# Kernel tuning notes

Measured on AMD Instinct MI355X. Metric: run time of the kernel, lower is better.

## Reference

```python
import jax, jax.numpy as jnp
import numpy as np

B, H, S, D = 1, 16, 4096, 64

def setup_inputs() -> dict:
    key = jax.random.key(0)
    kq, kk, kv = jax.random.split(key, 3)
    return {
        "query": jax.random.normal(kq, (B, H, S, D), dtype=jnp.float32),
        "key": jax.random.normal(kk, (B, H, S, D), dtype=jnp.float32),
        "value": jax.random.normal(kv, (B, H, S, D), dtype=jnp.float32),
    }

def reference(query, key, value):
    # qk: [B,H,S,S] materialized score matrix (unfused, as in original)
    qk = jnp.einsum("bhqd,bhkd->bhqk", query, key)
    attn = jax.nn.softmax(qk, axis=-1)
    # dropout_p = 0.0 -> identity
    out = jnp.einsum("bhqk,bhkd->bhqd", attn, value)
    return out
```

## Files before the change

kernel.cpp:

```cpp
#include <hip/hip_runtime.h>
#include <math.h>


#define HH 16
#define SS 4096
#define DDm 64
#define WAVES 8
#define QBW 32
#define QB (WAVES * QBW)
#define KB 64
#define NTL (SS / KB)
#define LDP 72

typedef __attribute__((ext_vector_type(2))) _Float16 half2_t;
typedef __attribute__((ext_vector_type(4))) _Float16 half4_t;
typedef __attribute__((ext_vector_type(8))) _Float16 half8_t;
typedef __attribute__((ext_vector_type(16))) float f32x16;

union H8 { half2_t h2[4]; half8_t v; };
union FU { float f; unsigned u; };
union HU { half2_t h; unsigned u; };

__device__ inline unsigned asu(float x){ FU c; c.f=x; return c.u; }
__device__ inline float    asf(unsigned x){ FU c; c.u=x; return c.f; }
__device__ inline unsigned h2u(half2_t x){ HU c; c.h=x; return c.u; }
__device__ inline half2_t  u2h(unsigned x){ HU c; c.u=x; return c.h; }
__device__ inline half2_t  pk2(float a, float b){ half2_t h; h[0]=(_Float16)a; h[1]=(_Float16)b; return h; }

#if __has_builtin(__builtin_amdgcn_permlane32_swap)
#define HAVE_PL32 1
typedef __attribute__((ext_vector_type(2))) unsigned uint2_t;
__device__ inline uint2_t pl32(unsigned a, unsigned b){
  return __builtin_amdgcn_permlane32_swap(a, b, false, false);
}
#endif

#if __has_builtin(__builtin_amdgcn_exp2f)
#define EXP2F(x) __builtin_amdgcn_exp2f(x)
#else
#define EXP2F(x) exp2f(x)
#endif
#define L2E 1.44269504088896f

#define WAITVM(n) asm volatile("s_waitcnt vmcnt(" #n ")" ::: "memory")

__device__ __forceinline__ void gload16(const void* g, void* l) {
  __builtin_amdgcn_global_load_lds(
      (const __attribute__((address_space(1))) unsigned int*)g,
      (__attribute__((address_space(3))) unsigned int*)l, 16, 0, 0);
}

__global__ __launch_bounds__(256)
void prepack(const float* __restrict__ K, const float* __restrict__ V,
             _Float16* __restrict__ Kh, _Float16* __restrict__ Vth) {
  const int g = blockIdx.x;
  const int tid = threadIdx.x;
  if (g < 2048) {
    const int gt = g * 256 + tid;
    const int dg = gt & 7, r = (gt >> 3) & 63, t = (gt >> 9) & 63, h = gt >> 15;
    const float* src = K + ((size_t)(h * SS + t * 64 + r)) * DDm + dg * 8;
    float4 a = *(const float4*)src;
    float4 b = *(const float4*)(src + 4);
    H8 w;
    w.h2[0] = pk2(a.x, a.y); w.h2[1] = pk2(a.z, a.w);
    w.h2[2] = pk2(b.x, b.y); w.h2[3] = pk2(b.z, b.w);
    *(half8_t*)(Kh + (size_t)(h * 64 + t) * 4096 + (dg * 64 + r) * 8) = w.v;
  } else {
    const int gt = (g - 2048) * 256 + tid;
    const int dr = gt & 63, kg = (gt >> 6) & 7, t = (gt >> 9) & 63, h = gt >> 15;
    const float* src = V + ((size_t)(h * SS + t * 64 + kg * 8)) * DDm + dr;
    H8 w;
#pragma unroll
    for (int j = 0; j < 4; ++j)
      w.h2[j] = pk2(src[(2 * j) * DDm], src[(2 * j + 1) * DDm]);
    *(half8_t*)(Vth + (size_t)(h * 64 + t) * 4096 + (kg * 64 + dr) * 8) = w.v;
  }
}

__global__ __launch_bounds__(512, 2)
void attn_main(const float* __restrict__ Q, const _Float16* __restrict__ Kh,
               const _Float16* __restrict__ Vth, float* __restrict__ O) {
  __shared__ __align__(16) _Float16 Kbuf[3][4096];
  __shared__ __align__(16) _Float16 Vbuf[3][4096];

  const int tid  = threadIdx.x;
  const int lane = tid & 63;
  const int lo5  = lane & 31;
  const int hi   = lane >> 5;
  const int wv   = tid >> 6;

  const int lid  = blockIdx.x;
  const int head = 2 * (lid & 7) + ((lid >> 3) & 1);
  const int qt   = lid >> 4;
  const int qbase = qt * QB + wv * QBW;
  const size_t hoff = (size_t)head * SS * DDm;

  H8 qf[4];
  {
    const float* qp = Q + hoff + (size_t)(qbase + lo5) * DDm;
#pragma unroll
    for (int ds = 0; ds < 4; ++ds) {
      float4 a = *(const float4*)(qp + 16 * ds + 8 * hi);
      float4 b = *(const float4*)(qp + 16 * ds + 8 * hi + 4);
      qf[ds].h2[0] = pk2(a.x, a.y); qf[ds].h2[1] = pk2(a.z, a.w);
      qf[ds].h2[2] = pk2(b.x, b.y); qf[ds].h2[3] = pk2(b.z, b.w);
    }
  }

  const _Float16* kt0 = Kh + (size_t)head * 64 * 4096;
  const _Float16* vt0 = Vth + (size_t)head * 64 * 4096;

  f32x16 acc[2];
#pragma unroll
  for (int nt = 0; nt < 2; ++nt)
#pragma unroll
    for (int r = 0; r < 16; ++r) acc[nt][r] = 0.f;
  float m_run = -INFINITY, l_run = 0.f;

  gload16(kt0 + (size_t)tid * 8, &Kbuf[0][wv * 512]);
  gload16(vt0 + (size_t)tid * 8, &Vbuf[0][wv * 512]);
  gload16(kt0 + 4096 + (size_t)tid * 8, &Kbuf[1][wv * 512]);
  gload16(vt0 + 4096 + (size_t)tid * 8, &Vbuf[1][wv * 512]);

  int bc = 0;
  for (int t = 0; t < NTL; ++t) {
    if (t < NTL - 1) { WAITVM(2); } else { WAITVM(0); }
    __builtin_amdgcn_s_barrier();
    __builtin_amdgcn_sched_barrier(0);
    if (t + 2 < NTL) {
      int bi = bc + 2; if (bi >= 3) bi -= 3;
      gload16(kt0 + (size_t)(t + 2) * 4096 + (size_t)tid * 8, &Kbuf[bi][wv * 512]);
      gload16(vt0 + (size_t)(t + 2) * 4096 + (size_t)tid * 8, &Vbuf[bi][wv * 512]);
    }

    half8_t kf[2][4];
#pragma unroll
    for (int s = 0; s < 2; ++s)
#pragma unroll
      for (int ds = 0; ds < 4; ++ds)
        kf[s][ds] = *(const half8_t*)&Kbuf[bc][((ds * 2 + hi) * 64 + 32 * s + lo5) * 8];
    half8_t vfr[2][2][2];
#pragma unroll
    for (int s = 0; s < 2; ++s)
#pragma unroll
      for (int sp = 0; sp < 2; ++sp)
#pragma unroll
        for (int nt = 0; nt < 2; ++nt)
          vfr[s][sp][nt] = *(const half8_t*)&Vbuf[bc][(((s * 2 + sp) * 2 + hi) * 64 + nt * 32 + lo5) * 8];

#pragma unroll
    for (int s = 0; s < 2; ++s) {
      f32x16 st;
#pragma unroll
      for (int r = 0; r < 16; ++r) st[r] = 0.f;
#pragma unroll
      for (int ds = 0; ds < 4; ++ds)
        st = __builtin_amdgcn_mfma_f32_32x32x16_f16(kf[s][ds], qf[ds].v, st, 0, 0, 0);

      float a0 = fmaxf(st[0], st[1]),   a1 = fmaxf(st[2], st[3]);
      float a2 = fmaxf(st[4], st[5]),   a3 = fmaxf(st[6], st[7]);
      float a4 = fmaxf(st[8], st[9]),   a5 = fmaxf(st[10], st[11]);
      float a6 = fmaxf(st[12], st[13]), a7 = fmaxf(st[14], st[15]);
      float b0 = fmaxf(a0, a1), b1 = fmaxf(a2, a3);
      float b2 = fmaxf(a4, a5), b3 = fmaxf(a6, a7);
      float tmax = fmaxf(fmaxf(b0, b1), fmaxf(b2, b3));
#if HAVE_PL32
      { uint2_t pr = pl32(asu(tmax), asu(tmax)); tmax = fmaxf(asf(pr[0]), asf(pr[1])); }
#else
      tmax = fmaxf(tmax, __shfl_xor(tmax, 32, 64));
#endif
      if (__any(tmax > m_run + 8.f)) {
        float mnew = fmaxf(m_run, tmax);
        float corr = EXP2F((m_run - mnew) * L2E);
        m_run = mnew; l_run *= corr;
#pragma unroll
        for (int r = 0; r < 16; ++r) {
          const int qr = (r & 3) + 8 * (r >> 2) + 4 * hi;
          float cf = asf(__builtin_amdgcn_ds_bpermute(qr << 2, asu(corr)));
          acc[0][r] *= cf; acc[1][r] *= cf;
        }
      }

      const float mt = m_run * L2E;
      float p[16];
      float s0 = 0.f, s1 = 0.f, s2 = 0.f, s3 = 0.f;
#pragma unroll
      for (int r = 0; r < 16; r += 4) {
        p[r]     = EXP2F(__builtin_fmaf(st[r],     L2E, -mt)); s0 += p[r];
        p[r + 1] = EXP2F(__builtin_fmaf(st[r + 1], L2E, -mt)); s1 += p[r + 1];
        p[r + 2] = EXP2F(__builtin_fmaf(st[r + 2], L2E, -mt)); s2 += p[r + 2];
        p[r + 3] = EXP2F(__builtin_fmaf(st[r + 3], L2E, -mt)); s3 += p[r + 3];
      }
      float lsum = (s0 + s1) + (s2 + s3);
#if HAVE_PL32
      { uint2_t pr = pl32(asu(lsum), asu(lsum)); lsum = asf(pr[0]) + asf(pr[1]); }
#else
      lsum += __shfl_xor(lsum, 32, 64);
#endif
      l_run += lsum;

      H8 pa[2];
#pragma unroll
      for (int step = 0; step < 2; ++step) {
        const int b = 8 * step;
        half2_t x0 = pk2(p[b + 0], p[b + 1]);
        half2_t x1 = pk2(p[b + 2], p[b + 3]);
        half2_t y0 = pk2(p[b + 4], p[b + 5]);
        half2_t y1 = pk2(p[b + 6], p[b + 7]);
#if HAVE_PL32
        uint2_t sA = pl32(h2u(x0), h2u(y0));
        uint2_t sB = pl32(h2u(x1), h2u(y1));
        pa[step].h2[0] = u2h(sA[0]); pa[step].h2[1] = u2h(sB[0]);
        pa[step].h2[2] = u2h(sA[1]); pa[step].h2[3] = u2h(sB[1]);
#else
        half2_t sx0 = u2h(__shfl_xor(h2u(x0), 32, 64));
        half2_t sx1 = u2h(__shfl_xor(h2u(x1), 32, 64));
        half2_t sy0 = u2h(__shfl_xor(h2u(y0), 32, 64));
        half2_t sy1 = u2h(__shfl_xor(h2u(y1), 32, 64));
        pa[step].h2[0] = hi ? sy0 : x0;  pa[step].h2[1] = hi ? sy1 : x1;
        pa[step].h2[2] = hi ? y0 : sx0;  pa[step].h2[3] = hi ? y1 : sx1;
#endif
      }
#pragma unroll
      for (int step = 0; step < 2; ++step)
#pragma unroll
        for (int nt = 0; nt < 2; ++nt)
          acc[nt] = __builtin_amdgcn_mfma_f32_32x32x16_f16(pa[step].v, vfr[s][step][nt], acc[nt], 0, 0, 0);
    }

    bc += 1; if (bc >= 3) bc = 0;
  }

  const float invl = 1.f / l_run;
#pragma unroll
  for (int r = 0; r < 16; ++r) {
    const int qr = (r & 3) + 8 * (r >> 2) + 4 * hi;
    float il = asf(__builtin_amdgcn_ds_bpermute(qr << 2, asu(invl)));
    float* op = O + hoff + (size_t)(qbase + qr) * DDm + lo5;
    op[0]  = acc[0][r] * il;
    op[32] = acc[1][r] * il;
  }
}

__global__ __launch_bounds__(512, 2)
void attn_fwd_fb(const float* __restrict__ Q, const float* __restrict__ K,
                 const float* __restrict__ V, float* __restrict__ O) {
  __shared__ __align__(16) _Float16 Klds[2][KB][LDP];
  __shared__ __align__(16) _Float16 Vt  [2][DDm][LDP];

  const int tid  = threadIdx.x;
  const int lane = tid & 63;
  const int lo5  = lane & 31;
  const int hi   = lane >> 5;

  const int lid  = blockIdx.x;
  const int head = 2 * (lid & 7) + ((lid >> 3) & 1);
  const int qt   = lid >> 4;
  const int qbase = qt * QB + (tid >> 6) * QBW;
  const size_t hoff = (size_t)head * SS * DDm;

  H8 qf[4];
  {
    const float* qp = Q + hoff + (size_t)(qbase + lo5) * DDm;
#pragma unroll
    for (int ds = 0; ds < 4; ++ds) {
      float4 a = *(const float4*)(qp + 16 * ds + 8 * hi);
      float4 b = *(const float4*)(qp + 16 * ds + 8 * hi + 4);
      qf[ds].h2[0] = pk2(a.x, a.y); qf[ds].h2[1] = pk2(a.z, a.w);
      qf[ds].h2[2] = pk2(b.x, b.y); qf[ds].h2[3] = pk2(b.z, b.w);
    }
  }

  const int krow = tid >> 3, kc8 = (tid & 7) * 8;
  const int vd = tid & 63, vk8 = (tid >> 6) * 8;

  float4 ka, kb; float va[8];
  auto issue = [&](int t) {
    const float* kp = K + hoff + (size_t)(t * KB + krow) * DDm + kc8;
    ka = *(const float4*)kp;
    kb = *(const float4*)(kp + 4);
    const float* vp = V + hoff + (size_t)(t * KB + vk8) * DDm + vd;
#pragma unroll
    for (int j = 0; j < 8; ++j) va[j] = vp[j * DDm];
  };
  auto wstage = [&](int buf) {
    H8 kw;
    kw.h2[0] = pk2(ka.x, ka.y); kw.h2[1] = pk2(ka.z, ka.w);
    kw.h2[2] = pk2(kb.x, kb.y); kw.h2[3] = pk2(kb.z, kb.w);
    *(half8_t*)&Klds[buf][krow][kc8] = kw.v;
    H8 vw;
#pragma unroll
    for (int j = 0; j < 4; ++j) vw.h2[j] = pk2(va[2 * j], va[2 * j + 1]);
    *(half8_t*)&Vt[buf][vd][vk8] = vw.v;
  };

  f32x16 acc[2];
#pragma unroll
  for (int nt = 0; nt < 2; ++nt)
#pragma unroll
    for (int r = 0; r < 16; ++r) acc[nt][r] = 0.f;
  float m_run = -INFINITY, l_run = 0.f;

  issue(0); wstage(0); __syncthreads();

  for (int t = 0; t < NTL; ++t) {
    const int cur = t & 1;
    if (t + 1 < NTL) issue(t + 1);

#pragma unroll
    for (int s = 0; s < 2; ++s) {
      const int rs = 32 * s;
      f32x16 st;
#pragma unroll
      for (int r = 0; r < 16; ++r) st[r] = 0.f;
#pragma unroll
      for (int ds = 0; ds < 4; ++ds) {
        half8_t af = *(const half8_t*)&Klds[cur][rs + lo5][16 * ds + 8 * hi];
        st = __builtin_amdgcn_mfma_f32_32x32x16_f16(af, qf[ds].v, st, 0, 0, 0);
      }
      float tmax = st[0];
#pragma unroll
      for (int r = 1; r < 16; ++r) tmax = fmaxf(tmax, st[r]);
#if HAVE_PL32
      { uint2_t pr = pl32(asu(tmax), asu(tmax)); tmax = fmaxf(asf(pr[0]), asf(pr[1])); }
#else
      tmax = fmaxf(tmax, __shfl_xor(tmax, 32, 64));
#endif
      if (__any(tmax > m_run + 8.f)) {
        float mnew = fmaxf(m_run, tmax);
        float corr = __expf(m_run - mnew);
        m_run = mnew; l_run *= corr;
#pragma unroll
        for (int r = 0; r < 16; ++r) {
          const int qr = (r & 3) + 8 * (r >> 2) + 4 * hi;
          float cf = asf(__builtin_amdgcn_ds_bpermute(qr << 2, asu(corr)));
          acc[0][r] *= cf; acc[1][r] *= cf;
        }
      }
      float p[16]; float lsum = 0.f;
#pragma unroll
      for (int r = 0; r < 16; ++r) { p[r] = __expf(st[r] - m_run); lsum += p[r]; }
#if HAVE_PL32
      { uint2_t pr = pl32(asu(lsum), asu(lsum)); lsum = asf(pr[0]) + asf(pr[1]); }
#else
      lsum += __shfl_xor(lsum, 32, 64);
#endif
      l_run += lsum;
      H8 pa[2];
#pragma unroll
      for (int step = 0; step < 2; ++step) {
        const int b = 8 * step;
        half2_t x0 = pk2(p[b + 0], p[b + 1]);
        half2_t x1 = pk2(p[b + 2], p[b + 3]);
        half2_t y0 = pk2(p[b + 4], p[b + 5]);
        half2_t y1 = pk2(p[b + 6], p[b + 7]);
#if HAVE_PL32
        uint2_t sA = pl32(h2u(x0), h2u(y0));
        uint2_t sB = pl32(h2u(x1), h2u(y1));
        pa[step].h2[0] = u2h(sA[0]); pa[step].h2[1] = u2h(sB[0]);
        pa[step].h2[2] = u2h(sA[1]); pa[step].h2[3] = u2h(sB[1]);
#else
        half2_t sx0 = u2h(__shfl_xor(h2u(x0), 32, 64));
        half2_t sx1 = u2h(__shfl_xor(h2u(x1), 32, 64));
        half2_t sy0 = u2h(__shfl_xor(h2u(y0), 32, 64));
        half2_t sy1 = u2h(__shfl_xor(h2u(y1), 32, 64));
        pa[step].h2[0] = hi ? sy0 : x0;  pa[step].h2[1] = hi ? sy1 : x1;
        pa[step].h2[2] = hi ? y0 : sx0;  pa[step].h2[3] = hi ? y1 : sx1;
#endif
      }
#pragma unroll
      for (int step = 0; step < 2; ++step)
#pragma unroll
        for (int nt = 0; nt < 2; ++nt) {
          half8_t vb = *(const half8_t*)&Vt[cur][32 * nt + lo5][rs + 16 * step + 8 * hi];
          acc[nt] = __builtin_amdgcn_mfma_f32_32x32x16_f16(pa[step].v, vb, acc[nt], 0, 0, 0);
        }
    }

    __syncthreads();
    if (t + 1 < NTL) wstage((t + 1) & 1);
    __syncthreads();
  }

  const float invl = 1.f / l_run;
#pragma unroll
  for (int r = 0; r < 16; ++r) {
    const int qr = (r & 3) + 8 * (r >> 2) + 4 * hi;
    float il = asf(__builtin_amdgcn_ds_bpermute(qr << 2, asu(invl)));
    float* op = O + hoff + (size_t)(qbase + qr) * DDm + lo5;
    op[0]  = acc[0][r] * il;
    op[32] = acc[1][r] * il;
  }
}

extern "C" void kernel_launch(void* const* d_in, const int* in_sizes, int n_in,
                              void* d_out, int out_size, void* d_ws, size_t ws_size,
                              hipStream_t stream) {
  const float* Q = (const float*)d_in[0];
  const float* K = (const float*)d_in[1];
  const float* V = (const float*)d_in[2];
  float* O = (float*)d_out;
  const size_t need = (size_t)2 * HH * SS * DDm * sizeof(_Float16);
  if (ws_size >= need) {
    _Float16* Kh  = (_Float16*)d_ws;
    _Float16* Vth = Kh + (size_t)HH * SS * DDm;
    prepack<<<dim3(4096), dim3(256), 0, stream>>>(K, V, Kh, Vth);
    attn_main<<<dim3(256), dim3(512), 0, stream>>>(Q, Kh, Vth, O);
  } else {
    attn_fwd_fb<<<dim3(256), dim3(512), 0, stream>>>(Q, K, V, O);
  }
}
```

Before: 115.2 us.

## Load K/V fragments directly from global into registers, drop LDS staging

Removes the shared-memory triple buffer and barriers from the main attention kernel. Each wave now loads its K and V MFMA fragments straight from the prepacked global buffers into registers, double-buffered across tiles. Blocks shrink from 512 to 256 threads and the grid doubles to keep the same query coverage. Each wave reading the full K/V tiles itself multiplies global/L2 traffic, and holding two register buffers raises register pressure.

```diff
diff --git a/kernel.cpp b/kernel.cpp
--- a/kernel.cpp
+++ b/kernel.cpp
@@ -5,15 +5,11 @@
 #define HH 16
 #define SS 4096
 #define DDm 64
-#define WAVES 8
-#define QBW 32
-#define QB (WAVES * QBW)
 #define KB 64
 #define NTL (SS / KB)
 #define LDP 72
 
 typedef __attribute__((ext_vector_type(2))) _Float16 half2_t;
-typedef __attribute__((ext_vector_type(4))) _Float16 half4_t;
 typedef __attribute__((ext_vector_type(8))) _Float16 half8_t;
 typedef __attribute__((ext_vector_type(16))) float f32x16;
 
@@ -41,14 +37,6 @@
 #define EXP2F(x) exp2f(x)
 #endif
 #define L2E 1.44269504088896f
-
-#define WAITVM(n) asm volatile("s_waitcnt vmcnt(" #n ")" ::: "memory")
-
-__device__ __forceinline__ void gload16(const void* g, void* l) {
-  __builtin_amdgcn_global_load_lds(
-      (const __attribute__((address_space(1))) unsigned int*)g,
-      (__attribute__((address_space(3))) unsigned int*)l, 16, 0, 0);
-}
 
 __global__ __launch_bounds__(256)
 void prepack(const float* __restrict__ K, const float* __restrict__ V,
@@ -77,12 +65,9 @@
   }
 }
 
-__global__ __launch_bounds__(512, 2)
+__global__ __launch_bounds__(256, 2)
 void attn_main(const float* __restrict__ Q, const _Float16* __restrict__ Kh,
                const _Float16* __restrict__ Vth, float* __restrict__ O) {
-  __shared__ __align__(16) _Float16 Kbuf[3][4096];
-  __shared__ __align__(16) _Float16 Vbuf[3][4096];
-
   const int tid  = threadIdx.x;
   const int lane = tid & 63;
   const int lo5  = lane & 31;
@@ -92,7 +77,7 @@
   const int lid  = blockIdx.x;
   const int head = 2 * (lid & 7) + ((lid >> 3) & 1);
   const int qt   = lid >> 4;
-  const int qbase = qt * QB + wv * QBW;
+  const int qbase = qt * 128 + wv * 32;
   const size_t hoff = (size_t)head * SS * DDm;
 
   H8 qf[4];
@@ -107,8 +92,27 @@
     }
   }
 
-  const _Float16* kt0 = Kh + (size_t)head * 64 * 4096;
-  const _Float16* vt0 = Vth + (size_t)head * 64 * 4096;
+  const _Float16* ktb = Kh + (size_t)head * 64 * 4096 + (hi * 64 + lo5) * 8;
+  const _Float16* vtb = Vth + (size_t)head * 64 * 4096 + (hi * 64 + lo5) * 8;
+
+  auto loadK = [&](int t, half8_t (&k)[8]) {
+    const _Float16* p = ktb + (size_t)t * 4096;
+#pragma unroll
+    for (int s = 0; s < 2; ++s)
+#pragma unroll
+      for (int ds = 0; ds < 4; ++ds)
+        k[s * 4 + ds] = *(const half8_t*)(p + (ds * 128 + 32 * s) * 8);
+  };
+  auto loadV = [&](int t, half8_t (&v)[8]) {
+    const _Float16* p = vtb + (size_t)t * 4096;
+#pragma unroll
+    for (int s = 0; s < 2; ++s)
+#pragma unroll
+      for (int sp = 0; sp < 2; ++sp)
+#pragma unroll
+        for (int nt = 0; nt < 2; ++nt)
+          v[s * 4 + sp * 2 + nt] = *(const half8_t*)(p + ((s * 2 + sp) * 128 + nt * 32) * 8);
+  };
 
   f32x16 acc[2];
 #pragma unroll
@@ -117,37 +121,7 @@
     for (int r = 0; r < 16; ++r) acc[nt][r] = 0.f;
   float m_run = -INFINITY, l_run = 0.f;
 
-  gload16(kt0 + (size_t)tid * 8, &Kbuf[0][wv * 512]);
-  gload16(vt0 + (size_t)tid * 8, &Vbuf[0][wv * 512]);
-  gload16(kt0 + 4096 + (size_t)tid * 8, &Kbuf[1][wv * 512]);
-  gload16(vt0 + 4096 + (size_t)tid * 8, &Vbuf[1][wv * 512]);
-
-  int bc = 0;
-  for (int t = 0; t < NTL; ++t) {
-    if (t < NTL - 1) { WAITVM(2); } else { WAITVM(0); }
-    __builtin_amdgcn_s_barrier();
-    __builtin_amdgcn_sched_barrier(0);
-    if (t + 2 < NTL) {
-      int bi = bc + 2; if (bi >= 3) bi -= 3;
-      gload16(kt0 + (size_t)(t + 2) * 4096 + (size_t)tid * 8, &Kbuf[bi][wv * 512]);
-      gload16(vt0 + (size_t)(t + 2) * 4096 + (size_t)tid * 8, &Vbuf[bi][wv * 512]);
-    }
-
-    half8_t kf[2][4];
-#pragma unroll
-    for (int s = 0; s < 2; ++s)
-#pragma unroll
-      for (int ds = 0; ds < 4; ++ds)
-        kf[s][ds] = *(const half8_t*)&Kbuf[bc][((ds * 2 + hi) * 64 + 32 * s + lo5) * 8];
-    half8_t vfr[2][2][2];
-#pragma unroll
-    for (int s = 0; s < 2; ++s)
-#pragma unroll
-      for (int sp = 0; sp < 2; ++sp)
-#pragma unroll
-        for (int nt = 0; nt < 2; ++nt)
-          vfr[s][sp][nt] = *(const half8_t*)&Vbuf[bc][(((s * 2 + sp) * 2 + hi) * 64 + nt * 32 + lo5) * 8];
-
+  auto compute = [&](half8_t (&k)[8], half8_t (&v)[8]) {
 #pragma unroll
     for (int s = 0; s < 2; ++s) {
       f32x16 st;
@@ -155,7 +129,7 @@
       for (int r = 0; r < 16; ++r) st[r] = 0.f;
 #pragma unroll
       for (int ds = 0; ds < 4; ++ds)
-        st = __builtin_amdgcn_mfma_f32_32x32x16_f16(kf[s][ds], qf[ds].v, st, 0, 0, 0);
+        st = __builtin_amdgcn_mfma_f32_32x32x16_f16(k[s * 4 + ds], qf[ds].v, st, 0, 0, 0);
 
       float a0 = fmaxf(st[0], st[1]),   a1 = fmaxf(st[2], st[3]);
       float a2 = fmaxf(st[4], st[5]),   a3 = fmaxf(st[6], st[7]);
@@ -225,10 +199,17 @@
       for (int step = 0; step < 2; ++step)
 #pragma unroll
         for (int nt = 0; nt < 2; ++nt)
-          acc[nt] = __builtin_amdgcn_mfma_f32_32x32x16_f16(pa[step].v, vfr[s][step][nt], acc[nt], 0, 0, 0);
+          acc[nt] = __builtin_amdgcn_mfma_f32_32x32x16_f16(pa[step].v, v[s * 4 + step * 2 + nt], acc[nt], 0, 0, 0);
     }
-
-    bc += 1; if (bc >= 3) bc = 0;
+  };
+
+  half8_t kA[8], vA[8], kB[8], vB[8];
+  loadK(0, kA); loadV(0, vA);
+  for (int t = 0; t < NTL; t += 2) {
+    loadK(t + 1, kB); loadV(t + 1, vB);
+    compute(kA, vA);
+    if (t + 2 < NTL) { loadK(t + 2, kA); loadV(t + 2, vA); }
+    compute(kB, vB);
   }
 
   const float invl = 1.f / l_run;
@@ -256,7 +237,7 @@
   const int lid  = blockIdx.x;
   const int head = 2 * (lid & 7) + ((lid >> 3) & 1);
   const int qt   = lid >> 4;
-  const int qbase = qt * QB + (tid >> 6) * QBW;
+  const int qbase = qt * 256 + (tid >> 6) * 32;
   const size_t hoff = (size_t)head * SS * DDm;
 
   H8 qf[4];
@@ -405,7 +386,7 @@
     _Float16* Kh  = (_Float16*)d_ws;
     _Float16* Vth = Kh + (size_t)HH * SS * DDm;
     prepack<<<dim3(4096), dim3(256), 0, stream>>>(K, V, Kh, Vth);
-    attn_main<<<dim3(256), dim3(512), 0, stream>>>(Q, Kh, Vth, O);
+    attn_main<<<dim3(512), dim3(256), 0, stream>>>(Q, Kh, Vth, O);
   } else {
     attn_fwd_fb<<<dim3(256), dim3(512), 0, stream>>>(Q, K, V, O);
   }
```

Result: slower. 125.3 us (+8.8%).

## Split KV sequence across two blocks per query tile and merge partials

Applied to the files above, without the earlier changes.

Adds a split-KV (flash-decoding style) path where each query tile is handled by two blocks, each covering half the key/value sequence, writing unnormalized accumulators plus running max and sum to workspace. A new merge kernel combines the two halves with log-sum-exp rescaling. This doubles the grid from 256 to 512 blocks to fill more compute units, at the cost of an extra kernel launch and partial-result traffic through global memory. The fp32 fallback kernel is removed, so no path runs when the workspace is too small.

```diff
diff --git a/kernel.cpp b/kernel.cpp
--- a/kernel.cpp
+++ b/kernel.cpp
@@ -5,15 +5,12 @@
 #define HH 16
 #define SS 4096
 #define DDm 64
-#define WAVES 8
-#define QBW 32
-#define QB (WAVES * QBW)
 #define KB 64
 #define NTL (SS / KB)
+#define NTLH 32
 #define LDP 72
 
 typedef __attribute__((ext_vector_type(2))) _Float16 half2_t;
-typedef __attribute__((ext_vector_type(4))) _Float16 half4_t;
 typedef __attribute__((ext_vector_type(8))) _Float16 half8_t;
 typedef __attribute__((ext_vector_type(16))) float f32x16;
 
@@ -78,8 +75,9 @@
 }
 
 __global__ __launch_bounds__(512, 2)
-void attn_main(const float* __restrict__ Q, const _Float16* __restrict__ Kh,
-               const _Float16* __restrict__ Vth, float* __restrict__ O) {
+void attn_split(const float* __restrict__ Q, const _Float16* __restrict__ Kh,
+                const _Float16* __restrict__ Vth, float* __restrict__ Pacc,
+                float* __restrict__ Pml) {
   __shared__ __align__(16) _Float16 Kbuf[3][4096];
   __shared__ __align__(16) _Float16 Vbuf[3][4096];
 
@@ -91,8 +89,206 @@
 
   const int lid  = blockIdx.x;
   const int head = 2 * (lid & 7) + ((lid >> 3) & 1);
+  const int rest = lid >> 4;
+  const int qt   = rest & 15;
+  const int half = rest >> 4;
+  const int qbase = qt * 256 + wv * 32;
+  const size_t hoff = (size_t)head * SS * DDm;
+
+  H8 qf[4];
+  {
+    const float* qp = Q + hoff + (size_t)(qbase + lo5) * DDm;
+#pragma unroll
+    for (int ds = 0; ds < 4; ++ds) {
+      float4 a = *(const float4*)(qp + 16 * ds + 8 * hi);
+      float4 b = *(const float4*)(qp + 16 * ds + 8 * hi + 4);
+      qf[ds].h2[0] = pk2(a.x, a.y); qf[ds].h2[1] = pk2(a.z, a.w);
+      qf[ds].h2[2] = pk2(b.x, b.y); qf[ds].h2[3] = pk2(b.z, b.w);
+    }
+  }
+
+  const _Float16* kt0 = Kh + (size_t)head * 64 * 4096 + (size_t)half * NTLH * 4096;
+  const _Float16* vt0 = Vth + (size_t)head * 64 * 4096 + (size_t)half * NTLH * 4096;
+
+  f32x16 acc[2];
+#pragma unroll
+  for (int nt = 0; nt < 2; ++nt)
+#pragma unroll
+    for (int r = 0; r < 16; ++r) acc[nt][r] = 0.f;
+  float m_run = -INFINITY, l_run = 0.f;
+
+  gload16(kt0 + (size_t)tid * 8, &Kbuf[0][wv * 512]);
+  gload16(vt0 + (size_t)tid * 8, &Vbuf[0][wv * 512]);
+  gload16(kt0 + 4096 + (size_t)tid * 8, &Kbuf[1][wv * 512]);
+  gload16(vt0 + 4096 + (size_t)tid * 8, &Vbuf[1][wv * 512]);
+
+  int bc = 0;
+  for (int t = 0; t < NTLH; ++t) {
+    if (t < NTLH - 1) { WAITVM(2); } else { WAITVM(0); }
+    __builtin_amdgcn_s_barrier();
+    __builtin_amdgcn_sched_barrier(0);
+    if (t + 2 < NTLH) {
+      int bi = bc + 2; if (bi >= 3) bi -= 3;
+      gload16(kt0 + (size_t)(t + 2) * 4096 + (size_t)tid * 8, &Kbuf[bi][wv * 512]);
+      gload16(vt0 + (size_t)(t + 2) * 4096 + (size_t)tid * 8, &Vbuf[bi][wv * 512]);
+    }
+
+    half8_t kf[2][4];
+#pragma unroll
+    for (int s = 0; s < 2; ++s)
+#pragma unroll
+      for (int ds = 0; ds < 4; ++ds)
+        kf[s][ds] = *(const half8_t*)&Kbuf[bc][((ds * 2 + hi) * 64 + 32 * s + lo5) * 8];
+    half8_t vfr[2][2][2];
+#pragma unroll
+    for (int s = 0; s < 2; ++s)
+#pragma unroll
+      for (int sp = 0; sp < 2; ++sp)
+#pragma unroll
+        for (int nt = 0; nt < 2; ++nt)
+          vfr[s][sp][nt] = *(const half8_t*)&Vbuf[bc][(((s * 2 + sp) * 2 + hi) * 64 + nt * 32 + lo5) * 8];
+
+#pragma unroll
+    for (int s = 0; s < 2; ++s) {
+      f32x16 st;
+#pragma unroll
+      for (int r = 0; r < 16; ++r) st[r] = 0.f;
+#pragma unroll
+      for (int ds = 0; ds < 4; ++ds)
+        st = __builtin_amdgcn_mfma_f32_32x32x16_f16(kf[s][ds], qf[ds].v, st, 0, 0, 0);
+
+      float a0 = fmaxf(st[0], st[1]),   a1 = fmaxf(st[2], st[3]);
+      float a2 = fmaxf(st[4], st[5]),   a3 = fmaxf(st[6], st[7]);
+      float a4 = fmaxf(st[8], st[9]),   a5 = fmaxf(st[10], st[11]);
+      float a6 = fmaxf(st[12], st[13]), a7 = fmaxf(st[14], st[15]);
+      float b0 = fmaxf(a0, a1), b1 = fmaxf(a2, a3);
+      float b2 = fmaxf(a4, a5), b3 = fmaxf(a6, a7);
+      float tmax = fmaxf(fmaxf(b0, b1), fmaxf(b2, b3));
+#if HAVE_PL32
+      { uint2_t pr = pl32(asu(tmax), asu(tmax)); tmax = fmaxf(asf(pr[0]), asf(pr[1])); }
+#else
+      tmax = fmaxf(tmax, __shfl_xor(tmax, 32, 64));
+#endif
+      if (__any(tmax > m_run + 8.f)) {
+        float mnew = fmaxf(m_run, tmax);
+        float corr = EXP2F((m_run - mnew) * L2E);
+        m_run = mnew; l_run *= corr;
+#pragma unroll
+        for (int r = 0; r < 16; ++r) {
+          const int qr = (r & 3) + 8 * (r >> 2) + 4 * hi;
+          float cf = asf(__builtin_amdgcn_ds_bpermute(qr << 2, asu(corr)));
+          acc[0][r] *= cf; acc[1][r] *= cf;
+        }
+      }
+
+      const float mt = m_run * L2E;
+      float p[16];
+      float s0 = 0.f, s1 = 0.f, s2 = 0.f, s3 = 0.f;
+#pragma unroll
+      for (int r = 0; r < 16; r += 4) {
+        p[r]     = EXP2F(__builtin_fmaf(st[r],     L2E, -mt)); s0 += p[r];
+        p[r + 1] = EXP2F(__builtin_fmaf(st[r + 1], L2E, -mt)); s1 += p[r + 1];
+        p[r + 2] = EXP2F(__builtin_fmaf(st[r + 2], L2E, -mt)); s2 += p[r + 2];
+        p[r + 3] = EXP2F(__builtin_fmaf(st[r + 3], L2E, -mt)); s3 += p[r + 3];
+      }
+      float lsum = (s0 + s1) + (s2 + s3);
+#if HAVE_PL32
+      { uint2_t pr = pl32(asu(lsum), asu(lsum)); lsum = asf(pr[0]) + asf(pr[1]); }
+#else
+      lsum += __shfl_xor(lsum, 32, 64);
+#endif
+      l_run += lsum;
+
+      H8 pa[2];
+#pragma unroll
+      for (int step = 0; step < 2; ++step) {
+        const int b = 8 * step;
+        half2_t x0 = pk2(p[b + 0], p[b + 1]);
+        half2_t x1 = pk2(p[b + 2], p[b + 3]);
+        half2_t y0 = pk2(p[b + 4], p[b + 5]);
+        half2_t y1 = pk2(p[b + 6], p[b + 7]);
+#if HAVE_PL32
+        uint2_t sA = pl32(h2u(x0), h2u(y0));
+        uint2_t sB = pl32(h2u(x1), h2u(y1));
+        pa[step].h2[0] = u2h(sA[0]); pa[step].h2[1] = u2h(sB[0]);
+        pa[step].h2[2] = u2h(sA[1]); pa[step].h2[3] = u2h(sB[1]);
+#else
+        half2_t sx0 = u2h(__shfl_xor(h2u(x0), 32, 64));
+        half2_t sx1 = u2h(__shfl_xor(h2u(x1), 32, 64));
+        half2_t sy0 = u2h(__shfl_xor(h2u(y0), 32, 64));
+        half2_t sy1 = u2h(__shfl_xor(h2u(y1), 32, 64));
+        pa[step].h2[0] = hi ? sy0 : x0;  pa[step].h2[1] = hi ? sy1 : x1;
+        pa[step].h2[2] = hi ? y0 : sx0;  pa[step].h2[3] = hi ? y1 : sx1;
+#endif
+      }
+#pragma unroll
+      for (int step = 0; step < 2; ++step)
+#pragma unroll
+        for (int nt = 0; nt < 2; ++nt)
+          acc[nt] = __builtin_amdgcn_mfma_f32_32x32x16_f16(pa[step].v, vfr[s][step][nt], acc[nt], 0, 0, 0);
+    }
+
+    bc += 1; if (bc >= 3) bc = 0;
+  }
+
+  const int pidx = (head * 16 + qt) * 2 + half;
+  float* pa = Pacc + (size_t)pidx * 16384;
+#pragma unroll
+  for (int r = 0; r < 16; ++r) {
+    const int qr = (r & 3) + 8 * (r >> 2) + 4 * hi;
+    float* op = pa + (wv * 32 + qr) * 64 + lo5;
+    op[0]  = acc[0][r];
+    op[32] = acc[1][r];
+  }
+  if (hi == 0) {
+    Pml[(size_t)pidx * 512 + wv * 32 + lo5]       = m_run;
+    Pml[(size_t)pidx * 512 + 256 + wv * 32 + lo5] = l_run;
+  }
+}
+
+__global__ __launch_bounds__(256)
+void merge_halves(const float* __restrict__ Pacc, const float* __restrict__ Pml,
+                  float* __restrict__ O) {
+  const int e  = (blockIdx.x * 256 + threadIdx.x) * 4;
+  const int d4 = e & 63;
+  const int q  = (e >> 6) & 255;
+  const int p  = e >> 14;
+  const float m0 = Pml[(size_t)(p * 2) * 512 + q];
+  const float l0 = Pml[(size_t)(p * 2) * 512 + 256 + q];
+  const float m1 = Pml[(size_t)(p * 2 + 1) * 512 + q];
+  const float l1 = Pml[(size_t)(p * 2 + 1) * 512 + 256 + q];
+  const float m  = fmaxf(m0, m1);
+  const float e0 = EXP2F((m0 - m) * L2E);
+  const float e1 = EXP2F((m1 - m) * L2E);
+  const float inv = 1.f / (e0 * l0 + e1 * l1);
+  const float f0 = e0 * inv, f1 = e1 * inv;
+  float4 x0 = *(const float4*)(Pacc + (size_t)(p * 2) * 16384 + q * 64 + d4);
+  float4 x1 = *(const float4*)(Pacc + (size_t)(p * 2 + 1) * 16384 + q * 64 + d4);
+  float4 o;
+  o.x = x0.x * f0 + x1.x * f1;
+  o.y = x0.y * f0 + x1.y * f1;
+  o.z = x0.z * f0 + x1.z * f1;
+  o.w = x0.w * f0 + x1.w * f1;
+  const int head = p >> 4, qt = p & 15;
+  *(float4*)(O + ((size_t)head * SS + qt * 256 + q) * DDm + d4) = o;
+}
+
+__global__ __launch_bounds__(512, 2)
+void attn_full(const float* __restrict__ Q, const _Float16* __restrict__ Kh,
+               const _Float16* __restrict__ Vth, float* __restrict__ O) {
+  __shared__ __align__(16) _Float16 Kbuf[3][4096];
+  __shared__ __align__(16) _Float16 Vbuf[3][4096];
+
+  const int tid  = threadIdx.x;
+  const int lane = tid & 63;
+  const int lo5  = lane & 31;
+  const int hi   = lane >> 5;
+  const int wv   = tid >> 6;
+
+  const int lid  = blockIdx.x;
+  const int head = 2 * (lid & 7) + ((lid >> 3) & 1);
   const int qt   = lid >> 4;
-  const int qbase = qt * QB + wv * QBW;
+  const int qbase = qt * 256 + wv * 32;
   const size_t hoff = (size_t)head * SS * DDm;
 
   H8 qf[4];
@@ -242,157 +438,6 @@
   }
 }
 
-__global__ __launch_bounds__(512, 2)
-void attn_fwd_fb(const float* __restrict__ Q, const float* __restrict__ K,
-                 const float* __restrict__ V, float* __restrict__ O) {
-  __shared__ __align__(16) _Float16 Klds[2][KB][LDP];
-  __shared__ __align__(16) _Float16 Vt  [2][DDm][LDP];
-
-  const int tid  = threadIdx.x;
-  const int lane = tid & 63;
-  const int lo5  = lane & 31;
-  const int hi   = lane >> 5;
-
-  const int lid  = blockIdx.x;
-  const int head = 2 * (lid & 7) + ((lid >> 3) & 1);
-  const int qt   = lid >> 4;
-  const int qbase = qt * QB + (tid >> 6) * QBW;
-  const size_t hoff = (size_t)head * SS * DDm;
-
-  H8 qf[4];
-  {
-    const float* qp = Q + hoff + (size_t)(qbase + lo5) * DDm;
-#pragma unroll
-    for (int ds = 0; ds < 4; ++ds) {
-      float4 a = *(const float4*)(qp + 16 * ds + 8 * hi);
-      float4 b = *(const float4*)(qp + 16 * ds + 8 * hi + 4);
-      qf[ds].h2[0] = pk2(a.x, a.y); qf[ds].h2[1] = pk2(a.z, a.w);
-      qf[ds].h2[2] = pk2(b.x, b.y); qf[ds].h2[3] = pk2(b.z, b.w);
-    }
-  }
-
-  const int krow = tid >> 3, kc8 = (tid & 7) * 8;
-  const int vd = tid & 63, vk8 = (tid >> 6) * 8;
-
-  float4 ka, kb; float va[8];
-  auto issue = [&](int t) {
-    const float* kp = K + hoff + (size_t)(t * KB + krow) * DDm + kc8;
-    ka = *(const float4*)kp;
-    kb = *(const float4*)(kp + 4);
-    const float* vp = V + hoff + (size_t)(t * KB + vk8) * DDm + vd;
-#pragma unroll
-    for (int j = 0; j < 8; ++j) va[j] = vp[j * DDm];
-  };
-  auto wstage = [&](int buf) {
-    H8 kw;
-    kw.h2[0] = pk2(ka.x, ka.y); kw.h2[1] = pk2(ka.z, ka.w);
-    kw.h2[2] = pk2(kb.x, kb.y); kw.h2[3] = pk2(kb.z, kb.w);
-    *(half8_t*)&Klds[buf][krow][kc8] = kw.v;
-    H8 vw;
-#pragma unroll
-    for (int j = 0; j < 4; ++j) vw.h2[j] = pk2(va[2 * j], va[2 * j + 1]);
-    *(half8_t*)&Vt[buf][vd][vk8] = vw.v;
-  };
-
-  f32x16 acc[2];
-#pragma unroll
-  for (int nt = 0; nt < 2; ++nt)
-#pragma unroll
-    for (int r = 0; r < 16; ++r) acc[nt][r] = 0.f;
-  float m_run = -INFINITY, l_run = 0.f;
-
-  issue(0); wstage(0); __syncthreads();
-
-  for (int t = 0; t < NTL; ++t) {
-    const int cur = t & 1;
-    if (t + 1 < NTL) issue(t + 1);
-
-#pragma unroll
-    for (int s = 0; s < 2; ++s) {
-      const int rs = 32 * s;
-      f32x16 st;
-#pragma unroll
-      for (int r = 0; r < 16; ++r) st[r] = 0.f;
-#pragma unroll
-      for (int ds = 0; ds < 4; ++ds) {
-        half8_t af = *(const half8_t*)&Klds[cur][rs + lo5][16 * ds + 8 * hi];
-        st = __builtin_amdgcn_mfma_f32_32x32x16_f16(af, qf[ds].v, st, 0, 0, 0);
-      }
-      float tmax = st[0];
-#pragma unroll
-      for (int r = 1; r < 16; ++r) tmax = fmaxf(tmax, st[r]);
-#if HAVE_PL32
-      { uint2_t pr = pl32(asu(tmax), asu(tmax)); tmax = fmaxf(asf(pr[0]), asf(pr[1])); }
-#else
-      tmax = fmaxf(tmax, __shfl_xor(tmax, 32, 64));
-#endif
-      if (__any(tmax > m_run + 8.f)) {
-        float mnew = fmaxf(m_run, tmax);
-        float corr = __expf(m_run - mnew);
-        m_run = mnew; l_run *= corr;
-#pragma unroll
-        for (int r = 0; r < 16; ++r) {
-          const int qr = (r & 3) + 8 * (r >> 2) + 4 * hi;
-          float cf = asf(__builtin_amdgcn_ds_bpermute(qr << 2, asu(corr)));
-          acc[0][r] *= cf; acc[1][r] *= cf;
-        }
-      }
-      float p[16]; float lsum = 0.f;
-#pragma unroll
-      for (int r = 0; r < 16; ++r) { p[r] = __expf(st[r] - m_run); lsum += p[r]; }
-#if HAVE_PL32
-      { uint2_t pr = pl32(asu(lsum), asu(lsum)); lsum = asf(pr[0]) + asf(pr[1]); }
-#else
-      lsum += __shfl_xor(lsum, 32, 64);
-#endif
-      l_run += lsum;
-      H8 pa[2];
-#pragma unroll
-      for (int step = 0; step < 2; ++step) {
-        const int b = 8 * step;
-        half2_t x0 = pk2(p[b + 0], p[b + 1]);
-        half2_t x1 = pk2(p[b + 2], p[b + 3]);
-        half2_t y0 = pk2(p[b + 4], p[b + 5]);
-        half2_t y1 = pk2(p[b + 6], p[b + 7]);
-#if HAVE_PL32
-        uint2_t sA = pl32(h2u(x0), h2u(y0));
-        uint2_t sB = pl32(h2u(x1), h2u(y1));
-        pa[step].h2[0] = u2h(sA[0]); pa[step].h2[1] = u2h(sB[0]);
-        pa[step].h2[2] = u2h(sA[1]); pa[step].h2[3] = u2h(sB[1]);
-#else
-        half2_t sx0 = u2h(__shfl_xor(h2u(x0), 32, 64));
-        half2_t sx1 = u2h(__shfl_xor(h2u(x1), 32, 64));
-        half2_t sy0 = u2h(__shfl_xor(h2u(y0), 32, 64));
-        half2_t sy1 = u2h(__shfl_xor(h2u(y1), 32, 64));
-        pa[step].h2[0] = hi ? sy0 : x0;  pa[step].h2[1] = hi ? sy1 : x1;
-        pa[step].h2[2] = hi ? y0 : sx0;  pa[step].h2[3] = hi ? y1 : sx1;
-#endif
-      }
-#pragma unroll
-      for (int step = 0; step < 2; ++step)
-#pragma unroll
-        for (int nt = 0; nt < 2; ++nt) {
-          half8_t vb = *(const half8_t*)&Vt[cur][32 * nt + lo5][rs + 16 * step + 8 * hi];
-          acc[nt] = __builtin_amdgcn_mfma_f32_32x32x16_f16(pa[step].v, vb, acc[nt], 0, 0, 0);
-        }
-    }
-
-    __syncthreads();
-    if (t + 1 < NTL) wstage((t + 1) & 1);
-    __syncthreads();
-  }
-
-  const float invl = 1.f / l_run;
-#pragma unroll
-  for (int r = 0; r < 16; ++r) {
-    const int qr = (r & 3) + 8 * (r >> 2) + 4 * hi;
-    float il = asf(__builtin_amdgcn_ds_bpermute(qr << 2, asu(invl)));
-    float* op = O + hoff + (size_t)(qbase + qr) * DDm + lo5;
-    op[0]  = acc[0][r] * il;
-    op[32] = acc[1][r] * il;
-  }
-}
-
 extern "C" void kernel_launch(void* const* d_in, const int* in_sizes, int n_in,
                               void* d_out, int out_size, void* d_ws, size_t ws_size,
                               hipStream_t stream) {
@@ -400,13 +445,24 @@
   const float* K = (const float*)d_in[1];
   const float* V = (const float*)d_in[2];
   float* O = (float*)d_out;
-  const size_t need = (size_t)2 * HH * SS * DDm * sizeof(_Float16);
-  if (ws_size >= need) {
+
+  const size_t n_kv   = (size_t)HH * SS * DDm;
+  const size_t sz_pre = 2 * n_kv * sizeof(_Float16);
+  const size_t sz_acc = (size_t)512 * 16384 * 4;
+  const size_t sz_ml  = (size_t)512 * 512 * 4;
+
+  if (ws_size >= sz_pre + sz_acc + sz_ml) {
     _Float16* Kh  = (_Float16*)d_ws;
-    _Float16* Vth = Kh + (size_t)HH * SS * DDm;
+    _Float16* Vth = Kh + n_kv;
+    float* Pacc = (float*)((char*)d_ws + sz_pre);
+    float* Pml  = (float*)((char*)d_ws + sz_pre + sz_acc);
     prepack<<<dim3(4096), dim3(256), 0, stream>>>(K, V, Kh, Vth);
-    attn_main<<<dim3(256), dim3(512), 0, stream>>>(Q, Kh, Vth, O);
-  } else {
-    attn_fwd_fb<<<dim3(256), dim3(512), 0, stream>>>(Q, K, V, O);
-  }
-}
+    attn_split<<<dim3(512), dim3(512), 0, stream>>>(Q, Kh, Vth, Pacc, Pml);
+    merge_halves<<<dim3(4096), dim3(256), 0, stream>>>(Pacc, Pml, O);
+  } else if (ws_size >= sz_pre) {
+    _Float16* Kh  = (_Float16*)d_ws;
+    _Float16* Vth = Kh + n_kv;
+    prepack<<<dim3(4096), dim3(256), 0, stream>>>(K, V, Kh, Vth);
+    attn_full<<<dim3(256), dim3(512), 0, stream>>>(Q, Kh, Vth, O);
+  }
+}
```

New measurement: 131.5 us. +14.1%, slower.
